# Kernel optimization log

Hardware: AMD Instinct MI355X
Metric: run time of the kernel (lower is better)

The kernel has to match this reference:

```python
import jax, jax.numpy as jnp
import numpy as np

N = 50000   # nodes
E = 800000  # edges (avg degree 16)
D = 64      # feature dim (input_dim == hidden_dim == output_dim for num_layer=2)
BN_EPS = 1e-5


def setup_inputs() -> dict:
    key = jax.random.key(0)
    ks = jax.random.split(key, 8)
    def lin_w(k, fan_in, fan_out):
        return jax.random.normal(k, (fan_in, fan_out), jnp.float32) / np.sqrt(fan_in).astype(np.float32)
    inp = {
        "x": jax.random.normal(ks[0], (N, D), jnp.float32),
        "edge_index": jax.random.randint(ks[1], (2, E), 0, N),
    }
    ki = 2
    for l in range(2):
        for s in ("a", "b"):
            inp[f"w{l}{s}"] = lin_w(ks[ki], D, D)
            inp[f"b{l}{s}"] = jnp.zeros((D,), jnp.float32)
            inp[f"g{l}{s}"] = jnp.ones((D,), jnp.float32)   # BN gamma
            inp[f"be{l}{s}"] = jnp.zeros((D,), jnp.float32)  # BN beta
            ki += 1
    inp["lin_w"] = lin_w(ks[6], 2 * D, D)  # JK cat of 2 layers -> 2D, final lin -> D
    inp["lin_b"] = jnp.zeros((D,), jnp.float32)
    return inp


def _bn(h, g, b):
    # BatchNorm1d in training mode: batch statistics over the node axis
    m = h.mean(axis=0)
    v = h.var(axis=0)
    return (h - m) * jax.lax.rsqrt(v + BN_EPS) * g + b


def _gin(h, src, dst, w1, b1, g1, be1, w2, b2, g2, be2):
    # GINConv with eps=0: (1+eps)*x_i + sum_{j->i} x_j, then MLP(Lin-BN-ReLU-Lin-BN-ReLU)
    agg = jax.ops.segment_sum(h[src], dst, num_segments=N) + h
    h = jax.nn.relu(_bn(agg @ w1 + b1, g1, be1))
    return jax.nn.relu(_bn(h @ w2 + b2, g2, be2))


def reference(x, edge_index, w0a, b0a, g0a, be0a, w0b, b0b, g0b, be0b,
              w1a, b1a, g1a, be1a, w1b, b1b, g1b, be1b, lin_w, lin_b):
    src, dst = edge_index[0], edge_index[1]
    h1 = _gin(x, src, dst, w0a, b0a, g0a, be0a, w0b, b0b, g0b, be0b)
    h2 = _gin(h1, src, dst, w1a, b1a, g1a, be1a, w1b, b1b, g1b, be1b)
    # JumpingKnowledge 'cat' over the conv outputs (res[1:]), then final linear
    return jnp.concatenate([h1, h2], axis=1) @ lin_w + lin_b
```

## Files before the change

### kernel.cpp

```cpp
#include <hip/hip_runtime.h>
#include <hip/hip_bf16.h>

#define NN 50000
#define NE 800000
#define BN_EPS 1e-5f
#define CHUNK 4096
#define NCH 196
#define NBK 196

typedef __attribute__((ext_vector_type(4))) float f32x4;
typedef __attribute__((ext_vector_type(8))) short s16x8;
typedef __attribute__((ext_vector_type(4))) short s16x4;

__device__ __forceinline__ float bf2f(__hip_bfloat16 v) { return __bfloat162float(v); }
__device__ __forceinline__ float bs2f(short v) {
    unsigned u = ((unsigned)(unsigned short)v) << 16;
    return __builtin_bit_cast(float, u);
}
__device__ __forceinline__ short f2bs(float v) {
    __hip_bfloat16 b = __float2bfloat16(v);
    return __builtin_bit_cast(short, b);
}

__global__ void prep_k(const int* __restrict__ dst, int* __restrict__ part,
                       const float* __restrict__ x, __hip_bfloat16* __restrict__ Xb,
                       const float* __restrict__ w0a, const float* __restrict__ w0b,
                       const float* __restrict__ w1a, const float* __restrict__ w1b,
                       const float* __restrict__ lw,
                       short* __restrict__ Wt0a, short* __restrict__ Wt0b,
                       short* __restrict__ Wt1a, short* __restrict__ Wt1b,
                       short* __restrict__ Wtf) {
    int b = blockIdx.x, t = threadIdx.x;
    if (b < NCH) {
        __shared__ int c[256];
        c[t] = 0;
        __syncthreads();
        int base = b * CHUNK;
        int n = NE - base; if (n > CHUNK) n = CHUNK;
        for (int i = t; i < n; i += 256) atomicAdd(&c[dst[base + i] >> 8], 1);
        __syncthreads();
        part[b * 256 + t] = c[t];
    } else if (b < 196 + 3125) {
        int i = (b - 196) * 256 + t;
        if (i < NN * 16) {
            f32x4 v = *(const f32x4*)(x + (size_t)i * 4);
            s16x4 ov;
            #pragma unroll
            for (int j = 0; j < 4; j++) ov[j] = f2bs(v[j]);
            *(s16x4*)((short*)Xb + (size_t)i * 4) = ov;
        }
    } else {
        int wb = b - 3321;
        if (wb < 4) {
            const float* W = wb == 0 ? w0a : wb == 1 ? w0b : wb == 2 ? w1a : w1b;
            short* Wt = wb == 0 ? Wt0a : wb == 1 ? Wt0b : wb == 2 ? Wt1a : Wt1b;
            for (int e = t; e < 4096; e += 256) {
                int k = e >> 6, n = e & 63;
                Wt[n * 64 + k] = f2bs(W[e]);
            }
        } else {
            for (int e = t; e < 8192; e += 256) {
                int k = e >> 6, n = e & 63;
                Wtf[n * 128 + k] = f2bs(lw[e]);
            }
        }
    }
}

__global__ void bscan_k(const int* __restrict__ part, int* __restrict__ bbase,
                        int* __restrict__ bres, int* __restrict__ off,
                        float* __restrict__ sums) {
    __shared__ int s[256];
    int t = threadIdx.x;
    int v = 0;
    for (int c = 0; c < NCH; c++) v += part[c * 256 + t];
    s[t] = v;
    __syncthreads();
    for (int d = 1; d < 256; d <<= 1) {
        int u = (t >= d) ? s[t - d] : 0;
        __syncthreads();
        s[t] += u;
        __syncthreads();
    }
    int ex = s[t] - v;
    bbase[t] = ex;
    bres[t] = ex;
    if (t == 0) { bbase[256] = NE; off[NN] = NE; }
    sums[t] = 0.f; sums[256 + t] = 0.f;
}

__global__ void bscatter_k(const int* __restrict__ src, const int* __restrict__ dst,
                           int* __restrict__ bres, int* __restrict__ ebuf) {
    __shared__ int cnt[256], loff[256], lcur[256], gst[256], sc[256];
    __shared__ int packed[CHUNK];
    int t = threadIdx.x;
    cnt[t] = 0;
    __syncthreads();
    int base = blockIdx.x * CHUNK;
    int n = NE - base; if (n > CHUNK) n = CHUNK;
    for (int i = t; i < n; i += 256) atomicAdd(&cnt[dst[base + i] >> 8], 1);
    __syncthreads();
    sc[t] = cnt[t];
    __syncthreads();
    for (int d = 1; d < 256; d <<= 1) {
        int u = (t >= d) ? sc[t - d] : 0;
        __syncthreads();
        sc[t] += u;
        __syncthreads();
    }
    loff[t] = sc[t] - cnt[t];
    lcur[t] = loff[t];
    __syncthreads();
    for (int i = t; i < n; i += 256) {
        int d = dst[base + i];
        int b = d >> 8;
        int p = atomicAdd(&lcur[b], 1);
        packed[p] = src[base + i] | ((d & 255) << 16) | (b << 24);
    }
    __syncthreads();
    if (cnt[t]) gst[t] = atomicAdd(&bres[t], cnt[t]);
    __syncthreads();
    for (int i = t; i < n; i += 256) {
        int v = packed[i];
        int b = (v >> 24) & 255;
        ebuf[gst[b] + i - loff[b]] = v & 0xFFFFFF;
    }
}

__global__ void csr_k(const int* __restrict__ bbase, const int* __restrict__ ebuf,
                      int* __restrict__ off, int* __restrict__ adj) {
    __shared__ int cnt[256], loff[256], lcur[256], sc[256];
    int b = blockIdx.x, t = threadIdx.x;
    int s0 = bbase[b], s1 = bbase[b + 1];
    int n = s1 - s0;
    cnt[t] = 0;
    __syncthreads();
    for (int i = t; i < n; i += 256) atomicAdd(&cnt[(ebuf[s0 + i] >> 16) & 255], 1);
    __syncthreads();
    sc[t] = cnt[t];
    __syncthreads();
    for (int d = 1; d < 256; d <<= 1) {
        int u = (t >= d) ? sc[t - d] : 0;
        __syncthreads();
        sc[t] += u;
        __syncthreads();
    }
    loff[t] = sc[t] - cnt[t];
    lcur[t] = loff[t];
    int node = b * 256 + t;
    if (node < NN) off[node] = s0 + loff[t];
    __syncthreads();
    for (int i = t; i < n; i += 256) {
        int v = ebuf[s0 + i];
        int p = atomicAdd(&lcur[(v >> 16) & 255], 1);
        adj[s0 + p] = v & 0xFFFF;
    }
}

__global__ void ggemm_k(const __hip_bfloat16* __restrict__ X,
                        const int* __restrict__ off, const int* __restrict__ adj,
                        const short* __restrict__ Wt,
                        const float* __restrict__ bias,
                        float* __restrict__ T,
                        float* __restrict__ sums) {
    __shared__ float lsum[64], lssq[64];
    int t = threadIdx.x;
    if (t < 64) { lsum[t] = 0.f; lssq[t] = 0.f; }
    __syncthreads();
    int wv = t >> 6, L = t & 63;
    int m = L & 15, quad = L >> 4;
    int wrow = blockIdx.x * 64 + wv * 16;
    int node = wrow + m;
    if (node >= NN) node = NN - 1;
    const short* Xp = (const short*)X;

    const short* rp = Xp + (size_t)node * 64 + quad * 8;
    s16x8 sl = *(const s16x8*)rp;
    s16x8 shh = *(const s16x8*)(rp + 32);
    float aL[8], aH[8];
    #pragma unroll
    for (int j = 0; j < 8; j++) { aL[j] = bs2f(sl[j]); aH[j] = bs2f(shh[j]); }

    int s = off[node], e = off[node + 1];
    int p = s;
    for (; p + 8 <= e; p += 8) {
        int jx[8];
        #pragma unroll
        for (int q = 0; q < 8; q++) jx[q] = adj[p + q];
        s16x8 v[8], w[8];
        #pragma unroll
        for (int q = 0; q < 8; q++) {
            const short* r = Xp + (size_t)jx[q] * 64 + quad * 8;
            v[q] = *(const s16x8*)r;
            w[q] = *(const s16x8*)(r + 32);
        }
        #pragma unroll
        for (int j = 0; j < 8; j++) {
            float sv = ((bs2f(v[0][j]) + bs2f(v[1][j])) + (bs2f(v[2][j]) + bs2f(v[3][j])))
                     + ((bs2f(v[4][j]) + bs2f(v[5][j])) + (bs2f(v[6][j]) + bs2f(v[7][j])));
            float sw = ((bs2f(w[0][j]) + bs2f(w[1][j])) + (bs2f(w[2][j]) + bs2f(w[3][j])))
                     + ((bs2f(w[4][j]) + bs2f(w[5][j])) + (bs2f(w[6][j]) + bs2f(w[7][j])));
            aL[j] += sv;
            aH[j] += sw;
        }
    }
    if (p + 4 <= e) {
        int j0 = adj[p], j1 = adj[p + 1], j2 = adj[p + 2], j3 = adj[p + 3];
        const short* r0 = Xp + (size_t)j0 * 64 + quad * 8;
        const short* r1 = Xp + (size_t)j1 * 64 + quad * 8;
        const short* r2 = Xp + (size_t)j2 * 64 + quad * 8;
        const short* r3 = Xp + (size_t)j3 * 64 + quad * 8;
        s16x8 v0 = *(const s16x8*)r0, w0 = *(const s16x8*)(r0 + 32);
        s16x8 v1 = *(const s16x8*)r1, w1 = *(const s16x8*)(r1 + 32);
        s16x8 v2 = *(const s16x8*)r2, w2 = *(const s16x8*)(r2 + 32);
        s16x8 v3 = *(const s16x8*)r3, w3 = *(const s16x8*)(r3 + 32);
        #pragma unroll
        for (int j = 0; j < 8; j++) {
            aL[j] += (bs2f(v0[j]) + bs2f(v1[j])) + (bs2f(v2[j]) + bs2f(v3[j]));
            aH[j] += (bs2f(w0[j]) + bs2f(w1[j])) + (bs2f(w2[j]) + bs2f(w3[j]));
        }
        p += 4;
    }
    for (; p < e; p++) {
        int j0 = adj[p];
        const short* r0 = Xp + (size_t)j0 * 64 + quad * 8;
        s16x8 v0 = *(const s16x8*)r0, w0 = *(const s16x8*)(r0 + 32);
        #pragma unroll
        for (int j = 0; j < 8; j++) { aL[j] += bs2f(v0[j]); aH[j] += bs2f(w0[j]); }
    }

    s16x8 a0, a1;
    #pragma unroll
    for (int j = 0; j < 8; j++) { a0[j] = f2bs(aL[j]); a1[j] = f2bs(aH[j]); }

    f32x4 acc[4];
    #pragma unroll
    for (int nt = 0; nt < 4; nt++) {
        int n = nt * 16 + m;
        s16x8 b0 = *(const s16x8*)(Wt + n * 64 + quad * 8);
        s16x8 b1 = *(const s16x8*)(Wt + n * 64 + 32 + quad * 8);
        acc[nt] = (f32x4){0.f, 0.f, 0.f, 0.f};
        acc[nt] = __builtin_amdgcn_mfma_f32_16x16x32_bf16(a0, b0, acc[nt], 0, 0, 0);
        acc[nt] = __builtin_amdgcn_mfma_f32_16x16x32_bf16(a1, b1, acc[nt], 0, 0, 0);
    }
    #pragma unroll
    for (int nt = 0; nt < 4; nt++) {
        int col = nt * 16 + m;
        float bv = bias[col];
        float ps = 0.f, pq = 0.f;
        #pragma unroll
        for (int r = 0; r < 4; r++) {
            int orow = wrow + quad * 4 + r;
            if (orow < NN) {
                float v = acc[nt][r] + bv;
                T[(size_t)orow * 64 + col] = v;
                ps += v;
                pq += v * v;
            }
        }
        atomicAdd(&lsum[col], ps);
        atomicAdd(&lssq[col], pq);
    }
    __syncthreads();
    if (t < 64) {
        atomicAdd(&sums[t], lsum[t]);
        atomicAdd(&sums[64 + t], lssq[t]);
    }
}

__global__ void gemm_bn_k(const float* __restrict__ Tin,
                          const float* __restrict__ stats,
                          const float* __restrict__ g, const float* __restrict__ be,
                          const short* __restrict__ Wt,
                          const float* __restrict__ bias,
                          float* __restrict__ T,
                          float* __restrict__ sums) {
    __shared__ float sc[64], sh[64], lsum[64], lssq[64];
    int tid = threadIdx.x;
    if (tid < 64) {
        float mm = stats[tid] * (1.0f / NN);
        float var = stats[64 + tid] * (1.0f / NN) - mm * mm;
        if (var < 0.f) var = 0.f;
        float s = g[tid] * rsqrtf(var + BN_EPS);
        sc[tid] = s;
        sh[tid] = be[tid] - mm * s;
        lsum[tid] = 0.f; lssq[tid] = 0.f;
    }
    __syncthreads();
    int wv = tid >> 6, L = tid & 63;
    int m = L & 15, quad = L >> 4;
    int wrow = blockIdx.x * 64 + wv * 16;
    int arow = wrow + m;
    if (arow >= NN) arow = NN - 1;
    f32x4 t0 = *(const f32x4*)(Tin + (size_t)arow * 64 + quad * 8);
    f32x4 t1 = *(const f32x4*)(Tin + (size_t)arow * 64 + quad * 8 + 4);
    f32x4 t2 = *(const f32x4*)(Tin + (size_t)arow * 64 + 32 + quad * 8);
    f32x4 t3 = *(const f32x4*)(Tin + (size_t)arow * 64 + 32 + quad * 8 + 4);
    s16x8 a0, a1;
    #pragma unroll
    for (int j = 0; j < 4; j++) {
        int k0 = quad * 8 + j, k1 = quad * 8 + 4 + j;
        float u0 = t0[j] * sc[k0] + sh[k0]; a0[j]     = f2bs(u0 > 0.f ? u0 : 0.f);
        float u1 = t1[j] * sc[k1] + sh[k1]; a0[4 + j] = f2bs(u1 > 0.f ? u1 : 0.f);
        float u2 = t2[j] * sc[32 + k0] + sh[32 + k0]; a1[j]     = f2bs(u2 > 0.f ? u2 : 0.f);
        float u3 = t3[j] * sc[32 + k1] + sh[32 + k1]; a1[4 + j] = f2bs(u3 > 0.f ? u3 : 0.f);
    }
    f32x4 acc[4];
    #pragma unroll
    for (int nt = 0; nt < 4; nt++) {
        int n = nt * 16 + m;
        s16x8 b0 = *(const s16x8*)(Wt + n * 64 + quad * 8);
        s16x8 b1 = *(const s16x8*)(Wt + n * 64 + 32 + quad * 8);
        acc[nt] = (f32x4){0.f, 0.f, 0.f, 0.f};
        acc[nt] = __builtin_amdgcn_mfma_f32_16x16x32_bf16(a0, b0, acc[nt], 0, 0, 0);
        acc[nt] = __builtin_amdgcn_mfma_f32_16x16x32_bf16(a1, b1, acc[nt], 0, 0, 0);
    }
    #pragma unroll
    for (int nt = 0; nt < 4; nt++) {
        int col = nt * 16 + m;
        float bv = bias[col];
        float ps = 0.f, pq = 0.f;
        #pragma unroll
        for (int r = 0; r < 4; r++) {
            int orow = wrow + quad * 4 + r;
            if (orow < NN) {
                float v = acc[nt][r] + bv;
                T[(size_t)orow * 64 + col] = v;
                ps += v;
                pq += v * v;
            }
        }
        atomicAdd(&lsum[col], ps);
        atomicAdd(&lssq[col], pq);
    }
    __syncthreads();
    if (tid < 64) {
        atomicAdd(&sums[tid], lsum[tid]);
        atomicAdd(&sums[64 + tid], lssq[tid]);
    }
}

__global__ void bn_k(const float* __restrict__ T, const float* __restrict__ sums,
                     const float* __restrict__ g, const float* __restrict__ be,
                     __hip_bfloat16* __restrict__ Hb) {
    __shared__ float sc[64], sh[64];
    int tid = threadIdx.x;
    if (tid < 64) {
        float m = sums[tid] * (1.0f / NN);
        float var = sums[64 + tid] * (1.0f / NN) - m * m;
        if (var < 0.f) var = 0.f;
        float s = g[tid] * rsqrtf(var + BN_EPS);
        sc[tid] = s;
        sh[tid] = be[tid] - m * s;
    }
    __syncthreads();
    int i = blockIdx.x * 256 + tid;
    if (i < NN * 16) {
        int row = i >> 4, f = (i & 15) * 4;
        f32x4 v = *(const f32x4*)(T + (size_t)row * 64 + f);
        s16x4 ub;
        #pragma unroll
        for (int j = 0; j < 4; j++) {
            float w = v[j] * sc[f + j] + sh[f + j];
            ub[j] = f2bs(w > 0.f ? w : 0.f);
        }
        *(s16x4*)((short*)Hb + (size_t)row * 64 + f) = ub;
    }
}

__global__ void gemm_fin_k(const __hip_bfloat16* __restrict__ H1b,
                           const float* __restrict__ T2,
                           const float* __restrict__ stats,
                           const float* __restrict__ g, const float* __restrict__ be,
                           const short* __restrict__ Wtf,
                           const float* __restrict__ bias,
                           float* __restrict__ O) {
    __shared__ float sc[64], sh[64];
    int tid = threadIdx.x;
    if (tid < 64) {
        float mm = stats[tid] * (1.0f / NN);
        float var = stats[64 + tid] * (1.0f / NN) - mm * mm;
        if (var < 0.f) var = 0.f;
        float s = g[tid] * rsqrtf(var + BN_EPS);
        sc[tid] = s;
        sh[tid] = be[tid] - mm * s;
    }
    __syncthreads();
    int wv = tid >> 6, L = tid & 63;
    int m = L & 15, quad = L >> 4;
    int wrow = blockIdx.x * 64 + wv * 16;
    int arow = wrow + m;
    if (arow >= NN) arow = NN - 1;
    const short* Hp = (const short*)H1b;
    s16x8 a0 = *(const s16x8*)(Hp + (size_t)arow * 64 + quad * 8);
    s16x8 a1 = *(const s16x8*)(Hp + (size_t)arow * 64 + 32 + quad * 8);
    f32x4 t0 = *(const f32x4*)(T2 + (size_t)arow * 64 + quad * 8);
    f32x4 t1 = *(const f32x4*)(T2 + (size_t)arow * 64 + quad * 8 + 4);
    f32x4 t2 = *(const f32x4*)(T2 + (size_t)arow * 64 + 32 + quad * 8);
    f32x4 t3 = *(const f32x4*)(T2 + (size_t)arow * 64 + 32 + quad * 8 + 4);
    s16x8 a2, a3;
    #pragma unroll
    for (int j = 0; j < 4; j++) {
        int k0 = quad * 8 + j, k1 = quad * 8 + 4 + j;
        float u0 = t0[j] * sc[k0] + sh[k0]; a2[j]     = f2bs(u0 > 0.f ? u0 : 0.f);
        float u1 = t1[j] * sc[k1] + sh[k1]; a2[4 + j] = f2bs(u1 > 0.f ? u1 : 0.f);
        float u2 = t2[j] * sc[32 + k0] + sh[32 + k0]; a3[j]     = f2bs(u2 > 0.f ? u2 : 0.f);
        float u3 = t3[j] * sc[32 + k1] + sh[32 + k1]; a3[4 + j] = f2bs(u3 > 0.f ? u3 : 0.f);
    }
    f32x4 acc[4];
    #pragma unroll
    for (int nt = 0; nt < 4; nt++) {
        int n = nt * 16 + m;
        s16x8 b0 = *(const s16x8*)(Wtf + n * 128 + quad * 8);
        s16x8 b1 = *(const s16x8*)(Wtf + n * 128 + 32 + quad * 8);
        s16x8 b2 = *(const s16x8*)(Wtf + n * 128 + 64 + quad * 8);
        s16x8 b3 = *(const s16x8*)(Wtf + n * 128 + 96 + quad * 8);
        acc[nt] = (f32x4){0.f, 0.f, 0.f, 0.f};
        acc[nt] = __builtin_amdgcn_mfma_f32_16x16x32_bf16(a0, b0, acc[nt], 0, 0, 0);
        acc[nt] = __builtin_amdgcn_mfma_f32_16x16x32_bf16(a1, b1, acc[nt], 0, 0, 0);
        acc[nt] = __builtin_amdgcn_mfma_f32_16x16x32_bf16(a2, b2, acc[nt], 0, 0, 0);
        acc[nt] = __builtin_amdgcn_mfma_f32_16x16x32_bf16(a3, b3, acc[nt], 0, 0, 0);
    }
    #pragma unroll
    for (int nt = 0; nt < 4; nt++) {
        int col = nt * 16 + m;
        float bv = bias[col];
        #pragma unroll
        for (int r = 0; r < 4; r++) {
            int orow = wrow + quad * 4 + r;
            if (orow < NN) O[(size_t)orow * 64 + col] = acc[nt][r] + bv;
        }
    }
}

extern "C" void kernel_launch(void* const* d_in, const int* in_sizes, int n_in,
                              void* d_out, int out_size, void* d_ws, size_t ws_size,
                              hipStream_t stream) {
    const float* x   = (const float*)d_in[0];
    const int*   ei  = (const int*)d_in[1];
    const float* w0a = (const float*)d_in[2];
    const float* b0a = (const float*)d_in[3];
    const float* g0a = (const float*)d_in[4];
    const float* be0a= (const float*)d_in[5];
    const float* w0b = (const float*)d_in[6];
    const float* b0b = (const float*)d_in[7];
    const float* g0b = (const float*)d_in[8];
    const float* be0b= (const float*)d_in[9];
    const float* w1a = (const float*)d_in[10];
    const float* b1a = (const float*)d_in[11];
    const float* g1a = (const float*)d_in[12];
    const float* be1a= (const float*)d_in[13];
    const float* w1b = (const float*)d_in[14];
    const float* b1b = (const float*)d_in[15];
    const float* g1b = (const float*)d_in[16];
    const float* be1b= (const float*)d_in[17];
    const float* lw  = (const float*)d_in[18];
    const float* lb  = (const float*)d_in[19];
    float* out = (float*)d_out;
    (void)in_sizes; (void)n_in; (void)out_size; (void)ws_size;

    char* wsb = (char*)d_ws;
    size_t o = 0;
    auto alloc = [&](size_t bytes) -> char* {
        char* p = wsb + o;
        o += (bytes + 255) & ~(size_t)255;
        return p;
    };
    int* part = (int*)alloc(NCH * 256 * 4);
    float* sums = (float*)alloc(512 * 4);
    int* bbase = (int*)alloc(257 * 4);
    int* bres = (int*)alloc(256 * 4);
    int* off = (int*)alloc((NN + 1) * 4);
    int* adj = (int*)alloc(NE * 4);
    int* ebuf = (int*)alloc(NE * 4);
    __hip_bfloat16* Xb  = (__hip_bfloat16*)alloc((size_t)NN * 64 * 2);
    __hip_bfloat16* HCb = (__hip_bfloat16*)alloc((size_t)NN * 64 * 2);
    float* T  = (float*)alloc((size_t)NN * 64 * 4);
    float* T2 = (float*)alloc((size_t)NN * 64 * 4);
    short* Wt0a = (short*)alloc(4096 * 2);
    short* Wt0b = (short*)alloc(4096 * 2);
    short* Wt1a = (short*)alloc(4096 * 2);
    short* Wt1b = (short*)alloc(4096 * 2);
    short* Wtf  = (short*)alloc(8192 * 2);

    const int* src = ei;
    const int* dst = ei + NE;

    prep_k<<<3326, 256, 0, stream>>>(dst, part, x, Xb, w0a, w0b, w1a, w1b, lw,
                                     Wt0a, Wt0b, Wt1a, Wt1b, Wtf);
    bscan_k<<<1, 256, 0, stream>>>(part, bbase, bres, off, sums);
    bscatter_k<<<NCH, 256, 0, stream>>>(src, dst, bres, ebuf);
    csr_k<<<NBK, 256, 0, stream>>>(bbase, ebuf, off, adj);

    const int mgrid = (NN + 63) / 64;
    const int agrid = (NN * 16 + 255) / 256;

    ggemm_k<<<mgrid, 256, 0, stream>>>(Xb, off, adj, Wt0a, b0a, T, sums + 0);
    gemm_bn_k<<<mgrid, 256, 0, stream>>>(T, sums + 0, g0a, be0a, Wt0b, b0b, T2, sums + 128);
    bn_k<<<agrid, 256, 0, stream>>>(T2, sums + 128, g0b, be0b, HCb);

    ggemm_k<<<mgrid, 256, 0, stream>>>(HCb, off, adj, Wt1a, b1a, T, sums + 256);
    gemm_bn_k<<<mgrid, 256, 0, stream>>>(T, sums + 256, g1a, be1a, Wt1b, b1b, T2, sums + 384);

    gemm_fin_k<<<mgrid, 256, 0, stream>>>(HCb, T2, sums + 384, g1b, be1b, Wtf, lb, out);
}
```

Before: 318.6 us.

## Split each node's neighbor gather across two waves and merge via LDS

The fused gather+GEMM kernel now assigns two waves to each 16-node tile. Each wave sums half of every node's neighbor list, and the second wave's partial sums are added into the first through shared memory before the MFMA step. The grid doubles to cover 32 nodes per block. The goal is more memory-level parallelism in the latency-bound irregular gather, at the cost of an LDS round trip, an extra barrier, and half the waves sitting idle during the GEMM/epilogue.

```diff
diff --git a/kernel.cpp b/kernel.cpp
--- a/kernel.cpp
+++ b/kernel.cpp
@@ -164,47 +164,54 @@
                         float* __restrict__ T,
                         float* __restrict__ sums) {
     __shared__ float lsum[64], lssq[64];
+    __shared__ float pacc[2][16 * 68];
     int t = threadIdx.x;
     if (t < 64) { lsum[t] = 0.f; lssq[t] = 0.f; }
-    __syncthreads();
-    int wv = t >> 6, L = t & 63;
-    int m = L & 15, quad = L >> 4;
-    int wrow = blockIdx.x * 64 + wv * 16;
-    int node = wrow + m;
+    int w = t >> 6, pair = w >> 1, h = w & 1;
+    int L = t & 63, m = L & 15, quad = L >> 4;
+    int prow = blockIdx.x * 32 + pair * 16;
+    int node = prow + m;
     if (node >= NN) node = NN - 1;
     const short* Xp = (const short*)X;
 
-    const short* rp = Xp + (size_t)node * 64 + quad * 8;
-    s16x8 sl = *(const s16x8*)rp;
-    s16x8 shh = *(const s16x8*)(rp + 32);
     float aL[8], aH[8];
-    #pragma unroll
-    for (int j = 0; j < 8; j++) { aL[j] = bs2f(sl[j]); aH[j] = bs2f(shh[j]); }
-
-    int s = off[node], e = off[node + 1];
-    int p = s;
-    for (; p + 8 <= e; p += 8) {
+    int s0 = off[node], e0 = off[node + 1];
+    int mid = s0 + ((e0 - s0) >> 1);
+    int ps, pe;
+    if (h == 0) {
+        const short* rp = Xp + (size_t)node * 64 + quad * 8;
+        s16x8 sv = *(const s16x8*)rp;
+        s16x8 sw = *(const s16x8*)(rp + 32);
+        #pragma unroll
+        for (int j = 0; j < 8; j++) { aL[j] = bs2f(sv[j]); aH[j] = bs2f(sw[j]); }
+        ps = s0; pe = mid;
+    } else {
+        #pragma unroll
+        for (int j = 0; j < 8; j++) { aL[j] = 0.f; aH[j] = 0.f; }
+        ps = mid; pe = e0;
+    }
+
+    int p = ps;
+    for (; p + 8 <= pe; p += 8) {
         int jx[8];
         #pragma unroll
         for (int q = 0; q < 8; q++) jx[q] = adj[p + q];
-        s16x8 v[8], w[8];
+        s16x8 v[8], wv[8];
         #pragma unroll
         for (int q = 0; q < 8; q++) {
             const short* r = Xp + (size_t)jx[q] * 64 + quad * 8;
             v[q] = *(const s16x8*)r;
-            w[q] = *(const s16x8*)(r + 32);
+            wv[q] = *(const s16x8*)(r + 32);
         }
         #pragma unroll
         for (int j = 0; j < 8; j++) {
-            float sv = ((bs2f(v[0][j]) + bs2f(v[1][j])) + (bs2f(v[2][j]) + bs2f(v[3][j])))
-                     + ((bs2f(v[4][j]) + bs2f(v[5][j])) + (bs2f(v[6][j]) + bs2f(v[7][j])));
-            float sw = ((bs2f(w[0][j]) + bs2f(w[1][j])) + (bs2f(w[2][j]) + bs2f(w[3][j])))
-                     + ((bs2f(w[4][j]) + bs2f(w[5][j])) + (bs2f(w[6][j]) + bs2f(w[7][j])));
-            aL[j] += sv;
-            aH[j] += sw;
-        }
-    }
-    if (p + 4 <= e) {
+            aL[j] += ((bs2f(v[0][j]) + bs2f(v[1][j])) + (bs2f(v[2][j]) + bs2f(v[3][j])))
+                   + ((bs2f(v[4][j]) + bs2f(v[5][j])) + (bs2f(v[6][j]) + bs2f(v[7][j])));
+            aH[j] += ((bs2f(wv[0][j]) + bs2f(wv[1][j])) + (bs2f(wv[2][j]) + bs2f(wv[3][j])))
+                   + ((bs2f(wv[4][j]) + bs2f(wv[5][j])) + (bs2f(wv[6][j]) + bs2f(wv[7][j])));
+        }
+    }
+    if (p + 4 <= pe) {
         int j0 = adj[p], j1 = adj[p + 1], j2 = adj[p + 2], j3 = adj[p + 3];
         const short* r0 = Xp + (size_t)j0 * 64 + quad * 8;
         const short* r1 = Xp + (size_t)j1 * 64 + quad * 8;
@@ -221,45 +228,61 @@
         }
         p += 4;
     }
-    for (; p < e; p++) {
-        int j0 = adj[p];
-        const short* r0 = Xp + (size_t)j0 * 64 + quad * 8;
+    for (; p < pe; p++) {
+        const short* r0 = Xp + (size_t)adj[p] * 64 + quad * 8;
         s16x8 v0 = *(const s16x8*)r0, w0 = *(const s16x8*)(r0 + 32);
         #pragma unroll
         for (int j = 0; j < 8; j++) { aL[j] += bs2f(v0[j]); aH[j] += bs2f(w0[j]); }
     }
 
-    s16x8 a0, a1;
-    #pragma unroll
-    for (int j = 0; j < 8; j++) { a0[j] = f2bs(aL[j]); a1[j] = f2bs(aH[j]); }
-
-    f32x4 acc[4];
-    #pragma unroll
-    for (int nt = 0; nt < 4; nt++) {
-        int n = nt * 16 + m;
-        s16x8 b0 = *(const s16x8*)(Wt + n * 64 + quad * 8);
-        s16x8 b1 = *(const s16x8*)(Wt + n * 64 + 32 + quad * 8);
-        acc[nt] = (f32x4){0.f, 0.f, 0.f, 0.f};
-        acc[nt] = __builtin_amdgcn_mfma_f32_16x16x32_bf16(a0, b0, acc[nt], 0, 0, 0);
-        acc[nt] = __builtin_amdgcn_mfma_f32_16x16x32_bf16(a1, b1, acc[nt], 0, 0, 0);
-    }
-    #pragma unroll
-    for (int nt = 0; nt < 4; nt++) {
-        int col = nt * 16 + m;
-        float bv = bias[col];
-        float ps = 0.f, pq = 0.f;
-        #pragma unroll
-        for (int r = 0; r < 4; r++) {
-            int orow = wrow + quad * 4 + r;
-            if (orow < NN) {
-                float v = acc[nt][r] + bv;
-                T[(size_t)orow * 64 + col] = v;
-                ps += v;
-                pq += v * v;
+    if (h == 1) {
+        float* dstp = &pacc[pair][m * 68];
+        #pragma unroll
+        for (int j = 0; j < 8; j++) {
+            dstp[quad * 8 + j] = aL[j];
+            dstp[32 + quad * 8 + j] = aH[j];
+        }
+    }
+    __syncthreads();
+    if (h == 0) {
+        const float* srcp = &pacc[pair][m * 68];
+        #pragma unroll
+        for (int j = 0; j < 8; j++) {
+            aL[j] += srcp[quad * 8 + j];
+            aH[j] += srcp[32 + quad * 8 + j];
+        }
+        s16x8 a0, a1;
+        #pragma unroll
+        for (int j = 0; j < 8; j++) { a0[j] = f2bs(aL[j]); a1[j] = f2bs(aH[j]); }
+
+        f32x4 acc[4];
+        #pragma unroll
+        for (int nt = 0; nt < 4; nt++) {
+            int n = nt * 16 + m;
+            s16x8 b0 = *(const s16x8*)(Wt + n * 64 + quad * 8);
+            s16x8 b1 = *(const s16x8*)(Wt + n * 64 + 32 + quad * 8);
+            acc[nt] = (f32x4){0.f, 0.f, 0.f, 0.f};
+            acc[nt] = __builtin_amdgcn_mfma_f32_16x16x32_bf16(a0, b0, acc[nt], 0, 0, 0);
+            acc[nt] = __builtin_amdgcn_mfma_f32_16x16x32_bf16(a1, b1, acc[nt], 0, 0, 0);
+        }
+        #pragma unroll
+        for (int nt = 0; nt < 4; nt++) {
+            int col = nt * 16 + m;
+            float bv = bias[col];
+            float pss = 0.f, pq = 0.f;
+            #pragma unroll
+            for (int r = 0; r < 4; r++) {
+                int orow = prow + quad * 4 + r;
+                if (orow < NN) {
+                    float vv = acc[nt][r] + bv;
+                    T[(size_t)orow * 64 + col] = vv;
+                    pss += vv;
+                    pq += vv * vv;
+                }
             }
-        }
-        atomicAdd(&lsum[col], ps);
-        atomicAdd(&lssq[col], pq);
+            atomicAdd(&lsum[col], pss);
+            atomicAdd(&lssq[col], pq);
+        }
     }
     __syncthreads();
     if (t < 64) {
@@ -492,14 +515,15 @@
     bscatter_k<<<NCH, 256, 0, stream>>>(src, dst, bres, ebuf);
     csr_k<<<NBK, 256, 0, stream>>>(bbase, ebuf, off, adj);
 
+    const int ggrid = (NN + 31) / 32;
     const int mgrid = (NN + 63) / 64;
     const int agrid = (NN * 16 + 255) / 256;
 
-    ggemm_k<<<mgrid, 256, 0, stream>>>(Xb, off, adj, Wt0a, b0a, T, sums + 0);
+    ggemm_k<<<ggrid, 256, 0, stream>>>(Xb, off, adj, Wt0a, b0a, T, sums + 0);
     gemm_bn_k<<<mgrid, 256, 0, stream>>>(T, sums + 0, g0a, be0a, Wt0b, b0b, T2, sums + 128);
     bn_k<<<agrid, 256, 0, stream>>>(T2, sums + 128, g0b, be0b, HCb);
 
-    ggemm_k<<<mgrid, 256, 0, stream>>>(HCb, off, adj, Wt1a, b1a, T, sums + 256);
+    ggemm_k<<<ggrid, 256, 0, stream>>>(HCb, off, adj, Wt1a, b1a, T, sums + 256);
     gemm_bn_k<<<mgrid, 256, 0, stream>>>(T, sums + 256, g1a, be1a, Wt1b, b1b, T2, sums + 384);
 
     gemm_fin_k<<<mgrid, 256, 0, stream>>>(HCb, T2, sums + 384, g1b, be1b, Wtf, lb, out);
```

After: 343.2 us. 1.08x slower.
